# Kernel tuning notes

Measured on AMD Instinct MI355X. Metric: run time of the kernel, lower is better.

The kernel has to match this reference:

```python
import jax, jax.numpy as jnp
import numpy as np

B, C, H, W = 16, 512, 32, 32
HW = H * W  # == input_features == output_features for shapes to be consistent


def setup_inputs() -> dict:
    key = jax.random.key(0)
    k1, k2, k3 = jax.random.split(key, 3)
    node1 = jax.random.normal(k1, (B, C, H, W), dtype=jnp.float32)
    node2 = jax.random.normal(k2, (B, C, H, W), dtype=jnp.float32)
    # nn.Linear(input_features, output_features, bias=False).weight: [out, in]
    W_c = jax.random.normal(k3, (HW, HW), dtype=jnp.float32) * (1.0 / np.sqrt(HW))
    return {"node1": node1, "node2": node2, "W_c": W_c}


def reference(node1, node2, W_c):
    b, c, h, w = node1.shape
    hw = h * w
    n1 = node1.reshape(b, c, hw)  # [B, C, HW]
    n2 = node2.reshape(b, c, hw)  # [B, C, HW]
    # x = W_c(n1): Linear applies y = x @ W^T  -> [B, C, HW_out]
    x = jnp.einsum('bch,oh->bco', n1, W_c)
    # e = bmm(x.permute(0,2,1), n2): [B, HW_out, C] @ [B, C, HW] -> [B, HW_out, HW]
    e = jnp.einsum('bco,bch->boh', x, n2)
    a = jax.nn.softmax(e, axis=-1)  # softmax over last dim (HW of node2)
    # m = bmm(n2, a): [B, C, HW] @ [B, HW, HW] -> [B, C, HW]
    m = jnp.einsum('bck,bkj->bcj', n2, a)
    return m
```

## Files before the change

kernel.cpp:

```cpp
#include <hip/hip_runtime.h>
#include <math.h>


typedef _Float16 f16;
typedef _Float16 f16x8 __attribute__((ext_vector_type(8)));
typedef _Float16 f16x4 __attribute__((ext_vector_type(4)));
typedef float f32x4 __attribute__((ext_vector_type(4)));

#define WG_BARRIER() asm volatile("s_waitcnt lgkmcnt(0)\ns_barrier" ::: "memory")

__global__ __launch_bounds__(256) void prep(const float* __restrict__ n1,
                                            const float* __restrict__ Wc,
                                            const float* __restrict__ n2,
                                            f16* __restrict__ n1f, f16* __restrict__ Wf,
                                            f16* __restrict__ n2f, f16* __restrict__ n2t) {
    const int bid = blockIdx.x, tid = threadIdx.x;
    if (bid < 4608) {
        const float* s = (bid < 4096) ? n1 : Wc;
        f16* d = (bid < 4096) ? n1f : Wf;
        const size_t i = ((size_t)(bid < 4096 ? bid : bid - 4096) * 256 + tid) * 8;
        f32x4 a = *(const f32x4*)(s + i);
        f32x4 b = *(const f32x4*)(s + i + 4);
        f16x8 o;
        o[0] = (f16)a[0]; o[1] = (f16)a[1]; o[2] = (f16)a[2]; o[3] = (f16)a[3];
        o[4] = (f16)b[0]; o[5] = (f16)b[1]; o[6] = (f16)b[2]; o[7] = (f16)b[3];
        *(f16x8*)(d + i) = o;
        return;
    }
    const int id = bid - 4608;
    const int b = id >> 7;
    const int ry = (id & 127) >> 4;
    const int cx = id & 15;
    const float* S = n2 + (size_t)b * 512 * 1024;
    f16* Dn = n2f + (size_t)b * 512 * 1024;
    f16* Dt = n2t + (size_t)b * 1024 * 512;
    __shared__ f16 Ts[64 * 72];
    const int r0 = ry * 64, c0 = cx * 64;
    const int rr = tid >> 3, cc8 = (tid & 7) * 8;
#pragma unroll
    for (int h = 0; h < 2; ++h) {
        const int row = r0 + rr + 32 * h;
        const float* s = S + (size_t)row * 1024 + c0 + cc8;
        f32x4 a = *(const f32x4*)s, bq = *(const f32x4*)(s + 4);
        f16x8 o;
        o[0] = (f16)a[0]; o[1] = (f16)a[1]; o[2] = (f16)a[2]; o[3] = (f16)a[3];
        o[4] = (f16)bq[0]; o[5] = (f16)bq[1]; o[6] = (f16)bq[2]; o[7] = (f16)bq[3];
        *(f16x8*)&Ts[(rr + 32 * h) * 72 + cc8] = o;
        *(f16x8*)(Dn + (size_t)row * 1024 + c0 + cc8) = o;
    }
    __syncthreads();
    const int j = tid >> 2, k16 = (tid & 3) * 16;
    f16* d = Dt + (size_t)(c0 + j) * 512 + r0 + k16;
    f16x8 o0, o1;
#pragma unroll
    for (int i = 0; i < 8; ++i) {
        o0[i] = Ts[(k16 + i) * 72 + j];
        o1[i] = Ts[(k16 + 8 + i) * 72 + j];
    }
    *(f16x8*)d = o0;
    *(f16x8*)(d + 8) = o1;
}

__global__ __launch_bounds__(256) void stats_partial(const f16* __restrict__ Et,
                                                     float* __restrict__ Pm,
                                                     float* __restrict__ Ps) {
    const int b = blockIdx.x & 15, chunk = blockIdx.x >> 4;
    const int t = threadIdx.x;
    const f16* p = Et + (size_t)b * 1024 * 1024 + (size_t)chunk * 64 * 1024 + t * 4;
    float m[4] = {-3.0e38f, -3.0e38f, -3.0e38f, -3.0e38f};
    float s[4] = {0.f, 0.f, 0.f, 0.f};
#pragma unroll 4
    for (int j = 0; j < 64; ++j) {
        f16x4 v4 = *(const f16x4*)(p + (size_t)j * 1024);
#pragma unroll
        for (int c = 0; c < 4; ++c) {
            float v = (float)v4[c];
            float nm = fmaxf(m[c], v);
            s[c] = s[c] * __expf(m[c] - nm) + __expf(v - nm);
            m[c] = nm;
        }
    }
    f32x4 mo, so;
#pragma unroll
    for (int c = 0; c < 4; ++c) { mo[c] = m[c]; so[c] = s[c]; }
    *(f32x4*)(Pm + (size_t)(b * 16 + chunk) * 1024 + t * 4) = mo;
    *(f32x4*)(Ps + (size_t)(b * 16 + chunk) * 1024 + t * 4) = so;
}

__global__ __launch_bounds__(256) void stats_combine(const float* __restrict__ Pm,
                                                     const float* __restrict__ Ps,
                                                     float* __restrict__ Sc) {
    const int g = blockIdx.x * 256 + threadIdx.x;
    const int b = g >> 10, o = g & 1023;
    const float* pm = Pm + (size_t)b * 16 * 1024 + o;
    const float* ps = Ps + (size_t)b * 16 * 1024 + o;
    float M = -3.0e38f;
#pragma unroll
    for (int c = 0; c < 16; ++c) M = fmaxf(M, pm[c * 1024]);
    float S = 0.f;
#pragma unroll
    for (int c = 0; c < 16; ++c) S += ps[c * 1024] * __expf(pm[c * 1024] - M);
    Sc[g] = M + __logf(S);
}

#define GEMM_CORE_D2(NS)                                                                \
    f16x8 pa0 = *(const f16x8*)gAp, pb0 = *(const f16x8*)gBp;                           \
    *(f16x8*)wA0 = pa0; *(f16x8*)wB0 = pb0;                                             \
    f16x8 pa1 = *(const f16x8*)(gAp + 64), pb1 = *(const f16x8*)(gBp + 64);             \
    pa0 = *(const f16x8*)(gAp + 128); pb0 = *(const f16x8*)(gBp + 128);                 \
    WG_BARRIER();                                                                       \
    f32x4 acc[4][2] = {};                                                               \
_Pragma("unroll")                                                                       \
    for (int kb = 0; kb < (NS); ++kb) {                                                 \
        const f16* Ac = (const f16*)(SM + (kb & 1) * 8192);                             \
        const f16* Bc = (const f16*)(SM + 16384 + (kb & 1) * 8192);                     \
        f16x8 fa[4], fb[2];                                                             \
_Pragma("unroll")                                                                       \
        for (int u = 0; u < 4; ++u)                                                     \
            fa[u] = *(const f16x8*)&Ac[(wm + u * 16 + col) * 32 + quad * 8];            \
_Pragma("unroll")                                                                       \
        for (int v = 0; v < 2; ++v)                                                     \
            fb[v] = *(const f16x8*)&Bc[(wn + v * 16 + col) * 32 + quad * 8];            \
_Pragma("unroll")                                                                       \
        for (int u = 0; u < 4; ++u)                                                     \
_Pragma("unroll")                                                                       \
            for (int v = 0; v < 2; ++v)                                                 \
                acc[u][v] = __builtin_amdgcn_mfma_f32_16x16x32_f16(fa[u], fb[v],        \
                                                                   acc[u][v], 0, 0, 0);\
        if (kb + 1 < (NS)) {                                                            \
            char* dA = SM + ((kb + 1) & 1) * 8192 + off;                                \
            char* dB = SM + 16384 + ((kb + 1) & 1) * 8192 + off;                        \
            if ((kb & 1) == 0) {                                                        \
                *(f16x8*)dA = pa1; *(f16x8*)dB = pb1;                                   \
                if (kb + 3 < (NS)) {                                                    \
                    pa1 = *(const f16x8*)(gAp + (size_t)(kb + 3) * 64);                 \
                    pb1 = *(const f16x8*)(gBp + (size_t)(kb + 3) * 64);                 \
                }                                                                       \
            } else {                                                                    \
                *(f16x8*)dA = pa0; *(f16x8*)dB = pb0;                                   \
                if (kb + 3 < (NS)) {                                                    \
                    pa0 = *(const f16x8*)(gAp + (size_t)(kb + 3) * 64);                 \
                    pb0 = *(const f16x8*)(gBp + (size_t)(kb + 3) * 64);                 \
                }                                                                       \
            }                                                                           \
            WG_BARRIER();                                                               \
        }                                                                               \
    }

__global__ __launch_bounds__(512) void gemm1_nt_xt(const f16* __restrict__ A,
                                                   const f16* __restrict__ Bw,
                                                   f16* __restrict__ Xt) {
    const int M = 512, K = 1024;
    const int id = blockIdx.x;
    const int xcd = id & 7, loc = id >> 3;
    const int b = xcd * 2 + (loc >> 5);
    const int m0 = ((loc >> 3) & 3) * 128;
    const int n0 = (loc & 7) * 128;
    A += (size_t)b * M * K;
    Xt += (size_t)b * 1024 * M;
    __shared__ __attribute__((aligned(16))) char SM[34816];
    const int tid = threadIdx.x, lane = tid & 63, wave = tid >> 6;
    const int col = lane & 15, quad = lane >> 4;
    const int wm = (wave & 1) * 64, wn = (wave >> 1) * 32;
    const int off = wave * 1024 + lane * 16;
    const int srow = off >> 6, scolb = off & 63;
    const char* gAp = (const char*)A + (size_t)(m0 + srow) * K * 2 + scolb;
    const char* gBp = (const char*)Bw + (size_t)(n0 + srow) * K * 2 + scolb;
    char* wA0 = SM + off;
    char* wB0 = SM + 16384 + off;

    GEMM_CORE_D2(32)

    WG_BARRIER();
    f16* Tt = (f16*)SM;
#pragma unroll
    for (int u = 0; u < 4; ++u)
#pragma unroll
        for (int v = 0; v < 2; ++v) {
            f16x4 p;
#pragma unroll
            for (int r = 0; r < 4; ++r) p[r] = (f16)acc[u][v][r];
            *(f16x4*)&Tt[(wn + v * 16 + col) * 136 + wm + u * 16 + quad * 4] = p;
        }
    WG_BARRIER();
    const int j = tid >> 2, seg = (tid & 3) * 32;
    f16* dst = Xt + (size_t)(n0 + j) * M + m0 + seg;
#pragma unroll
    for (int c8 = 0; c8 < 32; c8 += 8)
        *(f16x8*)(dst + c8) = *(const f16x8*)&Tt[j * 136 + seg + c8];
}

__global__ __launch_bounds__(512) void gemm2_nt_et(const f16* __restrict__ A,
                                                   const f16* __restrict__ B,
                                                   f16* __restrict__ Et) {
    const int K = 512;
    const int id = blockIdx.x;
    const int xcd = id & 7, loc = id >> 3;
    const int b = xcd * 2 + (loc >> 6);
    const int m0 = ((loc >> 3) & 7) * 128;
    const int n0 = (loc & 7) * 128;
    A += (size_t)b * 1024 * K;
    B += (size_t)b * 1024 * K;
    Et += (size_t)b * 1024 * 1024;
    __shared__ __attribute__((aligned(16))) char SM[34816];
    const int tid = threadIdx.x, lane = tid & 63, wave = tid >> 6;
    const int col = lane & 15, quad = lane >> 4;
    const int wm = (wave & 1) * 64, wn = (wave >> 1) * 32;
    const int off = wave * 1024 + lane * 16;
    const int srow = off >> 6, scolb = off & 63;
    const char* gAp = (const char*)A + (size_t)(m0 + srow) * K * 2 + scolb;
    const char* gBp = (const char*)B + (size_t)(n0 + srow) * K * 2 + scolb;
    char* wA0 = SM + off;
    char* wB0 = SM + 16384 + off;

    GEMM_CORE_D2(16)

    WG_BARRIER();
    f16* Tt = (f16*)SM;
#pragma unroll
    for (int u = 0; u < 4; ++u)
#pragma unroll
        for (int v = 0; v < 2; ++v) {
            f16x4 p;
#pragma unroll
            for (int r = 0; r < 4; ++r) p[r] = (f16)acc[u][v][r];
            *(f16x4*)&Tt[(wn + v * 16 + col) * 136 + wm + u * 16 + quad * 4] = p;
        }
    WG_BARRIER();
    const int j = tid >> 2, seg = (tid & 3) * 32;
    f16* dst = Et + (size_t)(n0 + j) * 1024 + m0 + seg;
#pragma unroll
    for (int c8 = 0; c8 < 32; c8 += 8)
        *(f16x8*)(dst + c8) = *(const f16x8*)&Tt[j * 136 + seg + c8];
}

__global__ __launch_bounds__(512) void gemm3_nt_out(const f16* __restrict__ A,
                                                    const f16* __restrict__ Et,
                                                    const float* __restrict__ Sc,
                                                    float* __restrict__ C) {
    const int K = 1024, NS = 32;
    const int id = blockIdx.x;
    const int xcd = id & 7, loc = id >> 3;
    const int b = xcd * 2 + (loc >> 5);
    const int m0 = ((loc >> 3) & 3) * 128;
    const int n0 = (loc & 7) * 128;
    A += (size_t)b * 512 * K;
    Et += (size_t)b * 1024 * K;
    Sc += (size_t)b * 1024;
    C += (size_t)b * 512 * 1024;
    __shared__ __attribute__((aligned(16))) char SM[32768];
    const int tid = threadIdx.x, lane = tid & 63, wave = tid >> 6;
    const int col = lane & 15, quad = lane >> 4;
    const int wm = (wave & 1) * 64, wn = (wave >> 1) * 32;
    const int off = wave * 1024 + lane * 16;
    const int srow = off >> 6, scolb = off & 63;
    const char* gAp = (const char*)A + (size_t)(m0 + srow) * K * 2 + scolb;
    const char* gBp = (const char*)Et + (size_t)(n0 + srow) * K * 2 + scolb;
    const float* gSp = Sc + (scolb >> 1);
    char* wA0 = SM + off;
    char* wB0 = SM + 16384 + off;

    f16x8 ra = *(const f16x8*)gAp, rb = *(const f16x8*)gBp;
    f32x4 c0 = *(const f32x4*)gSp, c1 = *(const f32x4*)(gSp + 4);
    {
        f16x8 rbs;
#pragma unroll
        for (int i = 0; i < 4; ++i) rbs[i] = (f16)__expf((float)rb[i] - c0[i]);
#pragma unroll
        for (int i = 0; i < 4; ++i) rbs[4 + i] = (f16)__expf((float)rb[4 + i] - c1[i]);
        *(f16x8*)wA0 = ra;
        *(f16x8*)wB0 = rbs;
    }
    ra = *(const f16x8*)(gAp + 64);
    rb = *(const f16x8*)(gBp + 64);
    c0 = *(const f32x4*)(gSp + 32);
    c1 = *(const f32x4*)(gSp + 36);
    WG_BARRIER();
    f32x4 acc[4][2] = {};
#pragma unroll
    for (int kb = 0; kb < NS; ++kb) {
        const f16* Ac = (const f16*)(SM + (kb & 1) * 8192);
        const f16* Bc = (const f16*)(SM + 16384 + (kb & 1) * 8192);
        f16x8 fa[4], fb[2];
#pragma unroll
        for (int u = 0; u < 4; ++u)
            fa[u] = *(const f16x8*)&Ac[(wm + u * 16 + col) * 32 + quad * 8];
#pragma unroll
        for (int v = 0; v < 2; ++v)
            fb[v] = *(const f16x8*)&Bc[(wn + v * 16 + col) * 32 + quad * 8];
#pragma unroll
        for (int u = 0; u < 4; ++u)
#pragma unroll
            for (int v = 0; v < 2; ++v)
                acc[u][v] = __builtin_amdgcn_mfma_f32_16x16x32_f16(fa[u], fb[v],
                                                                   acc[u][v], 0, 0, 0);
        if (kb + 1 < NS) {
            char* dA = SM + ((kb + 1) & 1) * 8192 + off;
            char* dB = SM + 16384 + ((kb + 1) & 1) * 8192 + off;
            f16x8 rbs;
#pragma unroll
            for (int i = 0; i < 4; ++i) rbs[i] = (f16)__expf((float)rb[i] - c0[i]);
#pragma unroll
            for (int i = 0; i < 4; ++i) rbs[4 + i] = (f16)__expf((float)rb[4 + i] - c1[i]);
            *(f16x8*)dA = ra;
            *(f16x8*)dB = rbs;
            if (kb + 2 < NS) {
                ra = *(const f16x8*)(gAp + (size_t)(kb + 2) * 64);
                rb = *(const f16x8*)(gBp + (size_t)(kb + 2) * 64);
                c0 = *(const f32x4*)(gSp + (size_t)(kb + 2) * 32);
                c1 = *(const f32x4*)(gSp + (size_t)(kb + 2) * 32 + 4);
            }
            WG_BARRIER();
        }
    }

#pragma unroll
    for (int u = 0; u < 4; ++u)
#pragma unroll
        for (int v = 0; v < 2; ++v)
#pragma unroll
            for (int r = 0; r < 4; ++r)
                C[(size_t)(m0 + wm + u * 16 + quad * 4 + r) * 1024 + n0 + wn + v * 16 + col] =
                    acc[u][v][r];
}

extern "C" void kernel_launch(void* const* d_in, const int* in_sizes, int n_in,
                              void* d_out, int out_size, void* d_ws, size_t ws_size,
                              hipStream_t stream) {
    const float* n1 = (const float*)d_in[0];
    const float* n2 = (const float*)d_in[1];
    const float* Wc = (const float*)d_in[2];
    float* out = (float*)d_out;
    char* ws = (char*)d_ws;

    f16* n2t = (f16*)(ws);
    f16* Xt  = (f16*)(ws + (16u << 20));
    f16* Wf  = (f16*)(ws + (32u << 20));
    f16* Et  = (f16*)(ws + (32u << 20));
    f16* n1f = (f16*)(ws + (64u << 20));
    f16* n2f = (f16*)(ws + (80u << 20));
    float* Pm = (float*)(ws + (64u << 20));
    float* Ps = (float*)(ws + (65u << 20));
    float* Sc = (float*)(ws + (66u << 20));

    prep<<<6656, dim3(256), 0, stream>>>(n1, Wc, n2, n1f, Wf, n2f, n2t);
    gemm1_nt_xt<<<512, dim3(512), 0, stream>>>(n1f, Wf, Xt);
    gemm2_nt_et<<<1024, dim3(512), 0, stream>>>(Xt, n2t, Et);
    stats_partial<<<256, dim3(256), 0, stream>>>(Et, Pm, Ps);
    stats_combine<<<64, dim3(256), 0, stream>>>(Pm, Ps, Sc);
    gemm3_nt_out<<<512, dim3(512), 0, stream>>>(n2f, Et, Sc, out);
}
```

Baseline: 210.0 us.

## Pad GEMM LDS rows, deepen gemm3 prefetch, widen stats loads, use exp2

The GEMM LDS tiles now use an 80-byte row stride instead of 64 bytes, padding each row to cut bank conflicts on the fragment reads. gemm3 moves from a one-ahead to a two-ahead register prefetch of its global loads. Its fused exponent now uses exp2f with a log2e-scaled log-sum-exp, folded into an FMA. stats_partial loads 8 halves per thread over half the rows, producing 32 partials per batch; this doubles the partial buffers and the combine work and adds register pressure.

```diff
diff --git a/kernel.cpp b/kernel.cpp
--- a/kernel.cpp
+++ b/kernel.cpp
@@ -6,6 +6,8 @@
 typedef _Float16 f16x8 __attribute__((ext_vector_type(8)));
 typedef _Float16 f16x4 __attribute__((ext_vector_type(4)));
 typedef float f32x4 __attribute__((ext_vector_type(4)));
+
+#define L2E 1.442695040888963f
 
 #define WG_BARRIER() asm volatile("s_waitcnt lgkmcnt(0)\ns_barrier" ::: "memory")
 
@@ -65,26 +67,33 @@
                                                      float* __restrict__ Pm,
                                                      float* __restrict__ Ps) {
     const int b = blockIdx.x & 15, chunk = blockIdx.x >> 4;
-    const int t = threadIdx.x;
-    const f16* p = Et + (size_t)b * 1024 * 1024 + (size_t)chunk * 64 * 1024 + t * 4;
-    float m[4] = {-3.0e38f, -3.0e38f, -3.0e38f, -3.0e38f};
-    float s[4] = {0.f, 0.f, 0.f, 0.f};
+    const int half = threadIdx.x >> 7;
+    const int t = threadIdx.x & 127;
+    const f16* p = Et + (size_t)b * 1024 * 1024 +
+                   ((size_t)chunk * 64 + half * 32) * 1024 + t * 8;
+    float m[8], s[8];
+#pragma unroll
+    for (int c = 0; c < 8; ++c) { m[c] = -3.0e38f; s[c] = 0.f; }
 #pragma unroll 4
-    for (int j = 0; j < 64; ++j) {
-        f16x4 v4 = *(const f16x4*)(p + (size_t)j * 1024);
-#pragma unroll
-        for (int c = 0; c < 4; ++c) {
-            float v = (float)v4[c];
+    for (int j = 0; j < 32; ++j) {
+        f16x8 v8 = *(const f16x8*)(p + (size_t)j * 1024);
+#pragma unroll
+        for (int c = 0; c < 8; ++c) {
+            float v = (float)v8[c];
             float nm = fmaxf(m[c], v);
             s[c] = s[c] * __expf(m[c] - nm) + __expf(v - nm);
             m[c] = nm;
         }
     }
-    f32x4 mo, so;
-#pragma unroll
-    for (int c = 0; c < 4; ++c) { mo[c] = m[c]; so[c] = s[c]; }
-    *(f32x4*)(Pm + (size_t)(b * 16 + chunk) * 1024 + t * 4) = mo;
-    *(f32x4*)(Ps + (size_t)(b * 16 + chunk) * 1024 + t * 4) = so;
+    const int idx32 = b * 32 + chunk * 2 + half;
+    f32x4 mo0, mo1, so0, so1;
+#pragma unroll
+    for (int c = 0; c < 4; ++c) { mo0[c] = m[c]; mo1[c] = m[c + 4];
+                                  so0[c] = s[c]; so1[c] = s[c + 4]; }
+    float* pmo = Pm + (size_t)idx32 * 1024 + t * 8;
+    float* pso = Ps + (size_t)idx32 * 1024 + t * 8;
+    *(f32x4*)pmo = mo0; *(f32x4*)(pmo + 4) = mo1;
+    *(f32x4*)pso = so0; *(f32x4*)(pso + 4) = so1;
 }
 
 __global__ __launch_bounds__(256) void stats_combine(const float* __restrict__ Pm,
@@ -92,15 +101,15 @@
                                                      float* __restrict__ Sc) {
     const int g = blockIdx.x * 256 + threadIdx.x;
     const int b = g >> 10, o = g & 1023;
-    const float* pm = Pm + (size_t)b * 16 * 1024 + o;
-    const float* ps = Ps + (size_t)b * 16 * 1024 + o;
+    const float* pm = Pm + (size_t)b * 32 * 1024 + o;
+    const float* ps = Ps + (size_t)b * 32 * 1024 + o;
     float M = -3.0e38f;
 #pragma unroll
-    for (int c = 0; c < 16; ++c) M = fmaxf(M, pm[c * 1024]);
+    for (int c = 0; c < 32; ++c) M = fmaxf(M, pm[c * 1024]);
     float S = 0.f;
 #pragma unroll
-    for (int c = 0; c < 16; ++c) S += ps[c * 1024] * __expf(pm[c * 1024] - M);
-    Sc[g] = M + __logf(S);
+    for (int c = 0; c < 32; ++c) S += ps[c * 1024] * __expf(pm[c * 1024] - M);
+    Sc[g] = (M + __logf(S)) * L2E;
 }
 
 #define GEMM_CORE_D2(NS)                                                                \
@@ -112,15 +121,15 @@
     f32x4 acc[4][2] = {};                                                               \
 _Pragma("unroll")                                                                       \
     for (int kb = 0; kb < (NS); ++kb) {                                                 \
-        const f16* Ac = (const f16*)(SM + (kb & 1) * 8192);                             \
-        const f16* Bc = (const f16*)(SM + 16384 + (kb & 1) * 8192);                     \
+        const char* Ac = SM + (kb & 1) * 10240;                                         \
+        const char* Bc = SM + 20480 + (kb & 1) * 10240;                                 \
         f16x8 fa[4], fb[2];                                                             \
 _Pragma("unroll")                                                                       \
         for (int u = 0; u < 4; ++u)                                                     \
-            fa[u] = *(const f16x8*)&Ac[(wm + u * 16 + col) * 32 + quad * 8];            \
+            fa[u] = *(const f16x8*)(Ac + (wm + u * 16 + col) * 80 + quad * 16);         \
 _Pragma("unroll")                                                                       \
         for (int v = 0; v < 2; ++v)                                                     \
-            fb[v] = *(const f16x8*)&Bc[(wn + v * 16 + col) * 32 + quad * 8];            \
+            fb[v] = *(const f16x8*)(Bc + (wn + v * 16 + col) * 80 + quad * 16);         \
 _Pragma("unroll")                                                                       \
         for (int u = 0; u < 4; ++u)                                                     \
 _Pragma("unroll")                                                                       \
@@ -128,8 +137,8 @@
                 acc[u][v] = __builtin_amdgcn_mfma_f32_16x16x32_f16(fa[u], fb[v],        \
                                                                    acc[u][v], 0, 0, 0);\
         if (kb + 1 < (NS)) {                                                            \
-            char* dA = SM + ((kb + 1) & 1) * 8192 + off;                                \
-            char* dB = SM + 16384 + ((kb + 1) & 1) * 8192 + off;                        \
+            char* dA = SM + ((kb + 1) & 1) * 10240 + sOff;                              \
+            char* dB = SM + 20480 + ((kb + 1) & 1) * 10240 + sOff;                      \
             if ((kb & 1) == 0) {                                                        \
                 *(f16x8*)dA = pa1; *(f16x8*)dB = pb1;                                   \
                 if (kb + 3 < (NS)) {                                                    \
@@ -158,16 +167,16 @@
     const int n0 = (loc & 7) * 128;
     A += (size_t)b * M * K;
     Xt += (size_t)b * 1024 * M;
-    __shared__ __attribute__((aligned(16))) char SM[34816];
+    __shared__ __attribute__((aligned(16))) char SM[40960];
     const int tid = threadIdx.x, lane = tid & 63, wave = tid >> 6;
     const int col = lane & 15, quad = lane >> 4;
     const int wm = (wave & 1) * 64, wn = (wave >> 1) * 32;
-    const int off = wave * 1024 + lane * 16;
-    const int srow = off >> 6, scolb = off & 63;
+    const int srow = wave * 16 + (lane >> 2), scolb = (lane & 3) * 16;
+    const int sOff = srow * 80 + scolb;
     const char* gAp = (const char*)A + (size_t)(m0 + srow) * K * 2 + scolb;
     const char* gBp = (const char*)Bw + (size_t)(n0 + srow) * K * 2 + scolb;
-    char* wA0 = SM + off;
-    char* wB0 = SM + 16384 + off;
+    char* wA0 = SM + sOff;
+    char* wB0 = SM + 20480 + sOff;
 
     GEMM_CORE_D2(32)
 
@@ -202,16 +211,16 @@
     A += (size_t)b * 1024 * K;
     B += (size_t)b * 1024 * K;
     Et += (size_t)b * 1024 * 1024;
-    __shared__ __attribute__((aligned(16))) char SM[34816];
+    __shared__ __attribute__((aligned(16))) char SM[40960];
     const int tid = threadIdx.x, lane = tid & 63, wave = tid >> 6;
     const int col = lane & 15, quad = lane >> 4;
     const int wm = (wave & 1) * 64, wn = (wave >> 1) * 32;
-    const int off = wave * 1024 + lane * 16;
-    const int srow = off >> 6, scolb = off & 63;
+    const int srow = wave * 16 + (lane >> 2), scolb = (lane & 3) * 16;
+    const int sOff = srow * 80 + scolb;
     const char* gAp = (const char*)A + (size_t)(m0 + srow) * K * 2 + scolb;
     const char* gBp = (const char*)B + (size_t)(n0 + srow) * K * 2 + scolb;
-    char* wA0 = SM + off;
-    char* wB0 = SM + 16384 + off;
+    char* wA0 = SM + sOff;
+    char* wB0 = SM + 20480 + sOff;
 
     GEMM_CORE_D2(16)
 
@@ -248,46 +257,48 @@
     Et += (size_t)b * 1024 * K;
     Sc += (size_t)b * 1024;
     C += (size_t)b * 512 * 1024;
-    __shared__ __attribute__((aligned(16))) char SM[32768];
+    __shared__ __attribute__((aligned(16))) char SM[40960];
     const int tid = threadIdx.x, lane = tid & 63, wave = tid >> 6;
     const int col = lane & 15, quad = lane >> 4;
     const int wm = (wave & 1) * 64, wn = (wave >> 1) * 32;
-    const int off = wave * 1024 + lane * 16;
-    const int srow = off >> 6, scolb = off & 63;
+    const int srow = wave * 16 + (lane >> 2), scolb = (lane & 3) * 16;
+    const int sOff = srow * 80 + scolb;
     const char* gAp = (const char*)A + (size_t)(m0 + srow) * K * 2 + scolb;
     const char* gBp = (const char*)Et + (size_t)(n0 + srow) * K * 2 + scolb;
     const float* gSp = Sc + (scolb >> 1);
-    char* wA0 = SM + off;
-    char* wB0 = SM + 16384 + off;
-
-    f16x8 ra = *(const f16x8*)gAp, rb = *(const f16x8*)gBp;
-    f32x4 c0 = *(const f32x4*)gSp, c1 = *(const f32x4*)(gSp + 4);
+    char* wA0 = SM + sOff;
+    char* wB0 = SM + 20480 + sOff;
+
+    f16x8 pa0 = *(const f16x8*)gAp, pb0 = *(const f16x8*)gBp;
+    f32x4 c00 = *(const f32x4*)gSp, c01 = *(const f32x4*)(gSp + 4);
     {
         f16x8 rbs;
 #pragma unroll
-        for (int i = 0; i < 4; ++i) rbs[i] = (f16)__expf((float)rb[i] - c0[i]);
-#pragma unroll
-        for (int i = 0; i < 4; ++i) rbs[4 + i] = (f16)__expf((float)rb[4 + i] - c1[i]);
-        *(f16x8*)wA0 = ra;
+        for (int i = 0; i < 4; ++i)
+            rbs[i] = (f16)exp2f(fmaf((float)pb0[i], L2E, -c00[i]));
+#pragma unroll
+        for (int i = 0; i < 4; ++i)
+            rbs[4 + i] = (f16)exp2f(fmaf((float)pb0[4 + i], L2E, -c01[i]));
+        *(f16x8*)wA0 = pa0;
         *(f16x8*)wB0 = rbs;
     }
-    ra = *(const f16x8*)(gAp + 64);
-    rb = *(const f16x8*)(gBp + 64);
-    c0 = *(const f32x4*)(gSp + 32);
-    c1 = *(const f32x4*)(gSp + 36);
+    f16x8 pa1 = *(const f16x8*)(gAp + 64), pb1 = *(const f16x8*)(gBp + 64);
+    f32x4 c10 = *(const f32x4*)(gSp + 32), c11 = *(const f32x4*)(gSp + 36);
+    pa0 = *(const f16x8*)(gAp + 128); pb0 = *(const f16x8*)(gBp + 128);
+    c00 = *(const f32x4*)(gSp + 64); c01 = *(const f32x4*)(gSp + 68);
     WG_BARRIER();
     f32x4 acc[4][2] = {};
 #pragma unroll
     for (int kb = 0; kb < NS; ++kb) {
-        const f16* Ac = (const f16*)(SM + (kb & 1) * 8192);
-        const f16* Bc = (const f16*)(SM + 16384 + (kb & 1) * 8192);
+        const char* Ac = SM + (kb & 1) * 10240;
+        const char* Bc = SM + 20480 + (kb & 1) * 10240;
         f16x8 fa[4], fb[2];
 #pragma unroll
         for (int u = 0; u < 4; ++u)
-            fa[u] = *(const f16x8*)&Ac[(wm + u * 16 + col) * 32 + quad * 8];
+            fa[u] = *(const f16x8*)(Ac + (wm + u * 16 + col) * 80 + quad * 16);
 #pragma unroll
         for (int v = 0; v < 2; ++v)
-            fb[v] = *(const f16x8*)&Bc[(wn + v * 16 + col) * 32 + quad * 8];
+            fb[v] = *(const f16x8*)(Bc + (wn + v * 16 + col) * 80 + quad * 16);
 #pragma unroll
         for (int u = 0; u < 4; ++u)
 #pragma unroll
@@ -295,20 +306,39 @@
                 acc[u][v] = __builtin_amdgcn_mfma_f32_16x16x32_f16(fa[u], fb[v],
                                                                    acc[u][v], 0, 0, 0);
         if (kb + 1 < NS) {
-            char* dA = SM + ((kb + 1) & 1) * 8192 + off;
-            char* dB = SM + 16384 + ((kb + 1) & 1) * 8192 + off;
+            char* dA = SM + ((kb + 1) & 1) * 10240 + sOff;
+            char* dB = SM + 20480 + ((kb + 1) & 1) * 10240 + sOff;
             f16x8 rbs;
-#pragma unroll
-            for (int i = 0; i < 4; ++i) rbs[i] = (f16)__expf((float)rb[i] - c0[i]);
-#pragma unroll
-            for (int i = 0; i < 4; ++i) rbs[4 + i] = (f16)__expf((float)rb[4 + i] - c1[i]);
-            *(f16x8*)dA = ra;
-            *(f16x8*)dB = rbs;
-            if (kb + 2 < NS) {
-                ra = *(const f16x8*)(gAp + (size_t)(kb + 2) * 64);
-                rb = *(const f16x8*)(gBp + (size_t)(kb + 2) * 64);
-                c0 = *(const f32x4*)(gSp + (size_t)(kb + 2) * 32);
-                c1 = *(const f32x4*)(gSp + (size_t)(kb + 2) * 32 + 4);
+            if ((kb & 1) == 0) {
+#pragma unroll
+                for (int i = 0; i < 4; ++i)
+                    rbs[i] = (f16)exp2f(fmaf((float)pb1[i], L2E, -c10[i]));
+#pragma unroll
+                for (int i = 0; i < 4; ++i)
+                    rbs[4 + i] = (f16)exp2f(fmaf((float)pb1[4 + i], L2E, -c11[i]));
+                *(f16x8*)dA = pa1;
+                *(f16x8*)dB = rbs;
+                if (kb + 3 < NS) {
+                    pa1 = *(const f16x8*)(gAp + (size_t)(kb + 3) * 64);
+                    pb1 = *(const f16x8*)(gBp + (size_t)(kb + 3) * 64);
+                    c10 = *(const f32x4*)(gSp + (size_t)(kb + 3) * 32);
+                    c11 = *(const f32x4*)(gSp + (size_t)(kb + 3) * 32 + 4);
+                }
+            } else {
+#pragma unroll
+                for (int i = 0; i < 4; ++i)
+                    rbs[i] = (f16)exp2f(fmaf((float)pb0[i], L2E, -c00[i]));
+#pragma unroll
+                for (int i = 0; i < 4; ++i)
+                    rbs[4 + i] = (f16)exp2f(fmaf((float)pb0[4 + i], L2E, -c01[i]));
+                *(f16x8*)dA = pa0;
+                *(f16x8*)dB = rbs;
+                if (kb + 3 < NS) {
+                    pa0 = *(const f16x8*)(gAp + (size_t)(kb + 3) * 64);
+                    pb0 = *(const f16x8*)(gBp + (size_t)(kb + 3) * 64);
+                    c00 = *(const f32x4*)(gSp + (size_t)(kb + 3) * 32);
+                    c01 = *(const f32x4*)(gSp + (size_t)(kb + 3) * 32 + 4);
+                }
             }
             WG_BARRIER();
         }
@@ -340,8 +370,8 @@
     f16* n1f = (f16*)(ws + (64u << 20));
     f16* n2f = (f16*)(ws + (80u << 20));
     float* Pm = (float*)(ws + (64u << 20));
-    float* Ps = (float*)(ws + (65u << 20));
-    float* Sc = (float*)(ws + (66u << 20));
+    float* Ps = (float*)(ws + (66u << 20));
+    float* Sc = (float*)(ws + (68u << 20));
 
     prep<<<6656, dim3(256), 0, stream>>>(n1, Wc, n2, n1f, Wf, n2f, n2t);
     gemm1_nt_xt<<<512, dim3(512), 0, stream>>>(n1f, Wf, Xt);
```

Result: slower. 218.0 us (+3.8%).
